# Kernel optimization log

Measured on AMD Instinct MI355X. Metric: run time of the kernel, lower is better.

The kernel has to match this reference:

```python
import jax, jax.numpy as jnp
import numpy as np

N, C, SI, VI, H, R = 10000, 2, 128, 16, 4, 32
SH, VH = SI // H, VI // H  # 32, 4
EPS = 1e-8

def _vnorm(x, axis):
    # clamped L2 norm, matches _norm_no_nan
    return jnp.sqrt(jnp.clip(jnp.sum(x * x, axis=axis), EPS, None))

def _gvp_full(s, v, wh, ws_w, ws_b, wv, wsv_w, wsv_b):
    # GVP with activations=(silu, sigmoid), vector_gate=True, vi=vo
    vh = jnp.swapaxes(v, -1, -2) @ wh            # [..., 3, h]
    vn = _vnorm(vh, -2)                          # [..., h]
    so = jnp.concatenate([s, vn], -1) @ ws_w + ws_b
    vo = jnp.swapaxes(vh @ wv, -1, -2)           # [..., vo, 3]
    gate = jax.nn.sigmoid(jax.nn.sigmoid(so) @ wsv_w + wsv_b)
    return jax.nn.silu(so), vo * gate[..., None]

def setup_inputs():
    key = jax.random.key(0)
    ks = iter(jax.random.split(key, 40))
    def lin(i, o):
        return jax.random.normal(next(ks), (i, o), jnp.float32) / np.sqrt(i)
    def bias(o):
        return 0.02 * jax.random.normal(next(ks), (o,), jnp.float32)
    inp = {}
    inp['s'] = jax.random.normal(next(ks), (N, C, SI), jnp.float32)
    inp['v'] = jax.random.normal(next(ks), (N, C, VI, 3), jnp.float32)
    # weight_proj: GVP((SI,VI)->(R,0)), no activations; h_dim = max(VI,0) = VI
    inp['wp_wh'] = lin(VI, VI); inp['wp_ws_w'] = lin(VI + SI, R); inp['wp_ws_b'] = bias(R)
    # to_q/k/v: GVP((SI,VI)->(SI,VI)), silu/sigmoid, vector_gate; h_dim = VI
    for p in ('q', 'k', 'vv'):
        inp[p + '_wh'] = lin(VI, VI)
        inp[p + '_ws_w'] = lin(VI + SI, SI); inp[p + '_ws_b'] = bias(SI)
        inp[p + '_wv'] = lin(VI, VI)
        inp[p + '_wsv_w'] = lin(SI, VI); inp[p + '_wsv_b'] = bias(VI)
    # attn_gvp_long: GVP((2*SH, 2*VH) -> (1,0)), no activations; h_dim = 2*VH
    inp['attn_wh'] = lin(2 * VH, 2 * VH)
    inp['attn_ws_w'] = lin(2 * VH + 2 * SH, 1); inp['attn_ws_b'] = bias(1)
    return inp

def reference(s, v, wp_wh, wp_ws_w, wp_ws_b,
              q_wh, q_ws_w, q_ws_b, q_wv, q_wsv_w, q_wsv_b,
              k_wh, k_ws_w, k_ws_b, k_wv, k_wsv_w, k_wsv_b,
              vv_wh, vv_ws_w, vv_ws_b, vv_wv, vv_wsv_w, vv_wsv_b,
              attn_wh, attn_ws_w, attn_ws_b):
    n, c = s.shape[:2]
    # ---- Compress: softmax-pool N -> R anchors ----
    vh = jnp.swapaxes(v, -1, -2) @ wp_wh          # [N,C,3,VI]
    vn = _vnorm(vh, -2)                            # [N,C,VI]
    pw = jnp.concatenate([s, vn], -1) @ wp_ws_w + wp_ws_b  # [N,C,R]
    pw = jax.nn.softmax(pw, axis=0)                # softmax over nodes
    s_g = jnp.einsum('nca,ncs->acs', pw, s)        # [R,C,SI] (includes transpose(0,1))
    v_g = jnp.einsum('nca,ncvd->acvd', pw, v)      # [R,C,VI,3]
    # ---- q from nodes, k/v from anchors ----
    qs, qv = _gvp_full(s, v, q_wh, q_ws_w, q_ws_b, q_wv, q_wsv_w, q_wsv_b)
    ks, kv = _gvp_full(s_g, v_g, k_wh, k_ws_w, k_ws_b, k_wv, k_wsv_w, k_wsv_b)
    vs, vv_ = _gvp_full(s_g, v_g, vv_wh, vv_ws_w, vv_ws_b, vv_wv, vv_wsv_w, vv_wsv_b)
    qs = qs.reshape(n, c, H, SH); qv = qv.reshape(n, c, H, VH, 3)
    ks = ks.reshape(R, c, H, SH); kv = kv.reshape(R, c, H, VH, 3)
    vs = vs.reshape(R, c, H, SH); vv_ = vv_.reshape(R, c, H, VH, 3)
    # ---- attention GVP on cat(q, k): split weights instead of materializing concat ----
    wh_q, wh_k = attn_wh[:VH], attn_wh[VH:]        # wh @ cat(qv,kv) = qv@wh_q + kv@wh_k
    qh = jnp.swapaxes(qv, -1, -2) @ wh_q           # [N,C,H,3,2VH]
    kh = jnp.swapaxes(kv, -1, -2) @ wh_k           # [R,C,H,3,2VH]
    vn2 = _vnorm(qh[:, None] + kh[None], -2)       # [N,R,C,H,2VH]
    ws_q = attn_ws_w[:SH]; ws_k = attn_ws_w[SH:2 * SH]; ws_n = attn_ws_w[2 * SH:]
    e = (qs @ ws_q)[:, None] + (ks @ ws_k)[None] + vn2 @ ws_n + attn_ws_b  # [N,R,C,H,1]
    e = e[..., 0] / np.sqrt(SH)
    alpha = jax.nn.softmax(e, axis=1)              # softmax over anchors (dim=1)
    # ---- Broadcast: weighted sum of anchor values ----
    out_s = jnp.einsum('nrch,rchd->nchd', alpha, vs).reshape(n, c, SI)
    out_v = jnp.einsum('nrch,rchde->nchde', alpha, vv_).reshape(n, c, VI, 3)
    return out_s, out_v
```

## Files before the change

### kernel.cpp

```cpp
#include <hip/hip_runtime.h>
#include <hip/hip_bf16.h>


#define N_  10000
#define C_  2
#define SI_ 128
#define VI_ 16
#define H_  4
#define R_  32
#define SH_ 32
#define VH_ 4
#define NC_ (N_*C_)

typedef const float* __restrict__ fptr;

__device__ __forceinline__ float sigm(float x){ return 1.f/(1.f+__expf(-x)); }

#define OFF_LG   0
#define OFF_EQH  640000
#define OFF_SG   2640000
#define OFF_TKH  2651520
#define OFF_TEK  2657664
#define OFF_TVS  2657920
#define OFF_TVV  2666112

#define SGSTRIDE_ 180

__global__ __launch_bounds__(256) void kA(
    fptr s, fptr v,
    fptr wp_wh, fptr wp_ws_w, fptr wp_ws_b,
    fptr q_wh, fptr q_ws_w, fptr q_ws_b, fptr q_wv, fptr q_wsv_w, fptr q_wsv_b,
    fptr attn_wh, fptr attn_ws_w,
    float* __restrict__ pexp, float* __restrict__ eqh)
{
  __shared__ __align__(16) float ARENA[160*20];
  __shared__ __align__(16) float VVs[16*48];
  __shared__ __align__(16) float VHQ[16*48];
  __shared__ __align__(16) float SO[16*128];
  __shared__ __align__(16) float GATE[16*16];
  __shared__ __align__(16) float QV[16*48];
  float* const XT  = ARENA;
  float* const SIG = ARENA;

  const int tid  = threadIdx.x;
  const int row0 = blockIdx.x * 16;

  for (int idx = tid; idx < 16*128; idx += 256){
    int r = idx >> 7, j = idx & 127;
    XT[j*20 + r] = s[(row0+r)*128 + j];
  }
  for (int idx = tid; idx < 16*48; idx += 256){
    int r = idx / 48, k = idx - r*48;
    VVs[r*48 + k] = v[(row0+r)*48 + k];
  }
  __syncthreads();

  for (int t = tid; t < 512; t += 256){
    int r = t >> 5, ii = t & 31, path = ii >> 4, i = ii & 15;
    fptr wh = path ? wp_wh : q_wh;
    float h0=0.f, h1=0.f, h2=0.f;
    #pragma unroll
    for (int j = 0; j < 16; j++){
      float w = wh[j*16 + i];
      h0 = fmaf(VVs[r*48 + j*3 + 0], w, h0);
      h1 = fmaf(VVs[r*48 + j*3 + 1], w, h1);
      h2 = fmaf(VVs[r*48 + j*3 + 2], w, h2);
    }
    float vn = sqrtf(fmaxf(h0*h0 + h1*h1 + h2*h2, 1e-8f));
    if (!path){
      VHQ[r*48 +  0 + i] = h0;
      VHQ[r*48 + 16 + i] = h1;
      VHQ[r*48 + 32 + i] = h2;
      XT[(128+i)*20 + r] = vn;
    } else {
      XT[(144+i)*20 + r] = vn;
    }
  }
  __syncthreads();

  const int colA = tid & 127, rgA = tid >> 7;
  float acc[8];
  {
    float bqs = q_ws_b[colA];
    #pragma unroll
    for (int k = 0; k < 8; k++) acc[k] = bqs;
    #pragma unroll 4
    for (int j = 0; j < 144; j++){
      float w = q_ws_w[j*128 + colA];
      const float* xp = &XT[j*20 + rgA*8];
      float4 x0 = *(const float4*)xp;
      float4 x1 = *(const float4*)(xp + 4);
      acc[0] = fmaf(x0.x, w, acc[0]); acc[1] = fmaf(x0.y, w, acc[1]);
      acc[2] = fmaf(x0.z, w, acc[2]); acc[3] = fmaf(x0.w, w, acc[3]);
      acc[4] = fmaf(x1.x, w, acc[4]); acc[5] = fmaf(x1.y, w, acc[5]);
      acc[6] = fmaf(x1.z, w, acc[6]); acc[7] = fmaf(x1.w, w, acc[7]);
    }
  }
  {
    const int col = tid & 31, rg = tid >> 5;
    float bp = wp_ws_b[col];
    float a0 = bp, a1 = bp;
    #pragma unroll 4
    for (int j = 0; j < 144; j++){
      int jj = (j < 128) ? j : (j + 16);
      float w = wp_ws_w[j*32 + col];
      const float* xp = &XT[jj*20 + rg*2];
      a0 = fmaf(xp[0], w, a0);
      a1 = fmaf(xp[1], w, a1);
    }
    const int n = (row0 >> 1) + rg;
    pexp[(     col)*N_ + n] = __expf(a0);
    pexp[(32 + col)*N_ + n] = __expf(a1);
  }
  __syncthreads();

  #pragma unroll
  for (int k = 0; k < 8; k++){
    float so = acc[k];
    float sg_ = sigm(so);
    SIG[(rgA*8 + k)*128 + colA] = sg_;
    SO [(rgA*8 + k)*128 + colA] = so * sg_;
  }
  __syncthreads();

  {
    const int r = tid >> 4, g = tid & 15;
    float ga = q_wsv_b[g];
    #pragma unroll 8
    for (int o = 0; o < 128; o += 4){
      float4 s4 = *(const float4*)&SIG[r*128 + o];
      ga = fmaf(s4.x, q_wsv_w[(o+0)*16 + g], ga);
      ga = fmaf(s4.y, q_wsv_w[(o+1)*16 + g], ga);
      ga = fmaf(s4.z, q_wsv_w[(o+2)*16 + g], ga);
      ga = fmaf(s4.w, q_wsv_w[(o+3)*16 + g], ga);
    }
    GATE[r*16 + g] = sigm(ga);
  }
  if (tid < 64){
    const int r = tid >> 2, h = tid & 3;
    float e = 0.f;
    #pragma unroll
    for (int t = 0; t < 32; t++)
      e = fmaf(SO[r*128 + h*32 + t], attn_ws_w[t], e);
    eqh[(row0 + r)*100 + h] = e;
  }
  __syncthreads();

  for (int t = tid; t < 16*48; t += 256){
    int r = t / 48, k = t - r*48, i = k / 3, d = k - i*3;
    float a = 0.f;
    #pragma unroll
    for (int j = 0; j < 16; j++)
      a = fmaf(VHQ[r*48 + d*16 + j], q_wv[j*16 + i], a);
    QV[r*48 + k] = a * GATE[r*16 + i];
  }
  __syncthreads();

  for (int t = tid; t < 16*96; t += 256){
    int r = t / 96, k = t - r*96;
    int h = k / 24, rem = k - h*24, d = rem >> 3, ee = rem & 7;
    float a = 0.f;
    #pragma unroll
    for (int i = 0; i < 4; i++)
      a = fmaf(QV[r*48 + (h*4 + i)*3 + d], attn_wh[i*8 + ee], a);
    eqh[(row0 + r)*100 + 8 + k] = a;
  }
}

__global__ __launch_bounds__(256) void kAccum(const float* __restrict__ pexp,
                                              fptr s, fptr v,
                                              float* __restrict__ sg)
{
  const int b = blockIdx.x;
  const int c = b & 1, ah = (b >> 1) & 1, chunk = b >> 2;
  const int n0 = chunk * 50;
  const int tid = threadIdx.x;
  const int ag = tid >> 6, dl = tid & 63;
  const int abase = ah*16 + ag*4;

  const float* pb = pexp + (c*32 + abase)*N_;
  float acc[4][3] = {};
  float dn[4] = {};

  #pragma unroll 2
  for (int n = n0; n < n0 + 50; n++){
    const int rc = n*2 + c;
    float pw[4];
    #pragma unroll
    for (int aa = 0; aa < 4; aa++){
      pw[aa] = pb[aa*N_ + n];
      dn[aa] += pw[aa];
    }
    #pragma unroll
    for (int dd = 0; dd < 3; dd++){
      int d = dl + 64*dd;
      if (d < 176){
        float xv = (d < 128) ? s[rc*128 + d] : v[rc*48 + d - 128];
        #pragma unroll
        for (int aa = 0; aa < 4; aa++)
          acc[aa][dd] = fmaf(pw[aa], xv, acc[aa][dd]);
      }
    }
  }
  #pragma unroll
  for (int aa = 0; aa < 4; aa++){
    const int base = (c*32 + abase + aa)*SGSTRIDE_;
    #pragma unroll
    for (int dd = 0; dd < 3; dd++){
      int d = dl + 64*dd;
      if (d < 176) atomicAdd(&sg[base + d], acc[aa][dd]);
    }
    if (dl == 0) atomicAdd(&sg[base + 176], dn[aa]);
  }
}

__global__ __launch_bounds__(256) void kSmall(
    const float* __restrict__ sg,
    fptr k_wh, fptr k_ws_w, fptr k_ws_b, fptr k_wv, fptr k_wsv_w, fptr k_wsv_b,
    fptr vv_wh, fptr vv_ws_w, fptr vv_ws_b, fptr vv_wv, fptr vv_wsv_w, fptr vv_wsv_b,
    fptr attn_wh, fptr attn_ws_w,
    float* __restrict__ tkh, float* __restrict__ tek,
    float* __restrict__ tvs, float* __restrict__ tvv)
{
  const int b = blockIdx.x, r = b >> 1, c = b & 1;
  const int tid = threadIdx.x;
  __shared__ float X[176];
  __shared__ float VN[2][16];
  __shared__ float VH[2][48];
  __shared__ float SOk[128], SOv[128];
  __shared__ float G[2][16];
  __shared__ float KV[48];

  if (tid < 176){
    const float* p = sg + (c*32 + r)*SGSTRIDE_;
    X[tid] = p[tid] / p[176];
  }
  __syncthreads();

  if (tid < 32){
    int path = tid >> 4, i = tid & 15;
    fptr wh = path ? vv_wh : k_wh;
    float h0=0.f, h1=0.f, h2=0.f;
    #pragma unroll
    for (int j = 0; j < 16; j++){
      float w = wh[j*16 + i];
      h0 = fmaf(X[128 + j*3 + 0], w, h0);
      h1 = fmaf(X[128 + j*3 + 1], w, h1);
      h2 = fmaf(X[128 + j*3 + 2], w, h2);
    }
    VH[path][ 0 + i] = h0; VH[path][16 + i] = h1; VH[path][32 + i] = h2;
    VN[path][i] = sqrtf(fmaxf(h0*h0 + h1*h1 + h2*h2, 1e-8f));
  }
  __syncthreads();

  {
    int path = tid >> 7, col = tid & 127;
    fptr W  = path ? vv_ws_w : k_ws_w;
    fptr Bb = path ? vv_ws_b : k_ws_b;
    float so = Bb[col];
    for (int j = 0; j < 128; j++) so = fmaf(X[j], W[j*128 + col], so);
    #pragma unroll
    for (int i = 0; i < 16; i++)  so = fmaf(VN[path][i], W[(128+i)*128 + col], so);
    (path ? SOv : SOk)[col] = so;
  }
  __syncthreads();

  if (tid < 32){
    int path = tid >> 4, g = tid & 15;
    fptr Wsv = path ? vv_wsv_w : k_wsv_w;
    fptr Bsv = path ? vv_wsv_b : k_wsv_b;
    const float* SOp = path ? SOv : SOk;
    float ga = Bsv[g];
    for (int o = 0; o < 128; o++)
      ga = fmaf(sigm(SOp[o]), Wsv[o*16 + g], ga);
    G[path][g] = sigm(ga);
  } else if (tid < 36){
    int h = tid - 32;
    float e = 0.f;
    #pragma unroll
    for (int t = 0; t < 32; t++){
      float so = SOk[h*32 + t];
      e = fmaf(so * sigm(so), attn_ws_w[32 + t], e);
    }
    tek[(r*2 + c)*4 + h] = e;
  } else if (tid >= 64 && tid < 192){
    int o = tid - 64;
    float so = SOv[o];
    tvs[(r*2 + c)*128 + o] = so * sigm(so);
  }
  __syncthreads();

  if (tid < 96){
    int path = tid / 48, k = tid % 48, i = k / 3, d = k - i*3;
    fptr Wv = path ? vv_wv : k_wv;
    float vo = 0.f;
    #pragma unroll
    for (int j = 0; j < 16; j++)
      vo = fmaf(VH[path][d*16 + j], Wv[j*16 + i], vo);
    float gv = vo * G[path][i];
    if (path == 0) KV[k] = gv;
    else {
      int h = i >> 2, ii = i & 3;
      tvv[(((r*2 + c)*4 + h)*4 + ii)*3 + d] = gv;
    }
  }
  __syncthreads();

  if (tid < 96){
    int h = tid / 24, rem = tid % 24, d = rem >> 3, ee = rem & 7;
    float a = 0.f;
    #pragma unroll
    for (int i = 0; i < 4; i++)
      a = fmaf(KV[(h*4 + i)*3 + d], attn_wh[(4 + i)*8 + ee], a);
    tkh[((r*2 + c)*4 + h)*24 + d*8 + ee] = a;
  }
}

__global__ __launch_bounds__(512, 1) void kAttn(
    const float* __restrict__ eqh,
    const float* __restrict__ tkh, const float* __restrict__ tek,
    const float* __restrict__ tvs, const float* __restrict__ tvv,
    fptr attn_ws_w, fptr attn_ws_b,
    float* __restrict__ out)
{
  __shared__ __align__(16) float KH[6144];
  __shared__ __align__(16) float EK[256];
  __shared__ __align__(16) float VS[256*36];
  __shared__ __align__(16) float VVt[3072];
  const int tid = threadIdx.x;

  for (int i = tid; i < 6144; i += 512) KH[i] = tkh[i];
  if (tid < 256) EK[tid] = tek[tid];
  for (int i = tid; i < 8192; i += 512){ int base = i >> 5, t = i & 31; VS[base*36 + t] = tvs[i]; }
  for (int i = tid; i < 3072; i += 512) VVt[i] = tvv[i];

  float wsn[8];
  #pragma unroll
  for (int ee = 0; ee < 8; ee++) wsn[ee] = attn_ws_w[64 + ee];
  const float wb = attn_ws_b[0];
  __syncthreads();

  const int row = blockIdx.x*128 + (tid >> 2);
  const int h = tid & 3;
  if (row < NC_){
    const int c = row & 1;
    const float eq = eqh[row*100 + h];
    float qh[24];
    {
      const float4* qp = (const float4*)&eqh[row*100 + 8 + h*24];
      #pragma unroll
      for (int k = 0; k < 6; k++){
        float4 t4 = qp[k];
        qh[k*4+0] = t4.x; qh[k*4+1] = t4.y; qh[k*4+2] = t4.z; qh[k*4+3] = t4.w;
      }
    }
    float4 accs4[8];
    float4 accv4[3];
    #pragma unroll
    for (int q = 0; q < 8; q++) accs4[q] = make_float4(0.f,0.f,0.f,0.f);
    #pragma unroll
    for (int q = 0; q < 3; q++) accv4[q] = make_float4(0.f,0.f,0.f,0.f);
    float den = 0.f;

    #pragma unroll
    for (int r = 0; r < 32; r++){
      const int base = (r*2 + c)*4 + h;
      const float* khp = &KH[base*24];
      float en = 0.f;
      #pragma unroll
      for (int ee = 0; ee < 8; ee++){
        float a0 = qh[ee]      + khp[ee];
        float a1 = qh[8 + ee]  + khp[8 + ee];
        float a2 = qh[16 + ee] + khp[16 + ee];
        en = fmaf(sqrtf(fmaxf(a0*a0 + a1*a1 + a2*a2, 1e-8f)), wsn[ee], en);
      }
      const float w = __expf((eq + EK[base] + en + wb) * 0.17677669529663687f);
      den += w;
      const float4* vp4 = (const float4*)&VS[base*36];
      #pragma unroll
      for (int q = 0; q < 8; q++){
        float4 t4 = vp4[q];
        accs4[q].x = fmaf(w, t4.x, accs4[q].x);
        accs4[q].y = fmaf(w, t4.y, accs4[q].y);
        accs4[q].z = fmaf(w, t4.z, accs4[q].z);
        accs4[q].w = fmaf(w, t4.w, accs4[q].w);
      }
      const float4* vv4 = (const float4*)&VVt[base*12];
      #pragma unroll
      for (int q = 0; q < 3; q++){
        float4 t4 = vv4[q];
        accv4[q].x = fmaf(w, t4.x, accv4[q].x);
        accv4[q].y = fmaf(w, t4.y, accv4[q].y);
        accv4[q].z = fmaf(w, t4.z, accv4[q].z);
        accv4[q].w = fmaf(w, t4.w, accv4[q].w);
      }
    }
    const float inv = 1.f / den;
    float4* po = (float4*)&out[row*128 + h*32];
    #pragma unroll
    for (int q = 0; q < 8; q++){
      float4 t4 = accs4[q];
      t4.x *= inv; t4.y *= inv; t4.z *= inv; t4.w *= inv;
      po[q] = t4;
    }
    float4* pv = (float4*)&out[NC_*128 + row*48 + h*12];
    #pragma unroll
    for (int q = 0; q < 3; q++){
      float4 t4 = accv4[q];
      t4.x *= inv; t4.y *= inv; t4.z *= inv; t4.w *= inv;
      pv[q] = t4;
    }
  }
}

extern "C" void kernel_launch(void* const* d_in, const int* in_sizes, int n_in,
                              void* d_out, int out_size, void* d_ws, size_t ws_size,
                              hipStream_t stream)
{
  fptr s        = (fptr)d_in[0];
  fptr v        = (fptr)d_in[1];
  fptr wp_wh    = (fptr)d_in[2];
  fptr wp_ws_w  = (fptr)d_in[3];
  fptr wp_ws_b  = (fptr)d_in[4];
  fptr q_wh     = (fptr)d_in[5];
  fptr q_ws_w   = (fptr)d_in[6];
  fptr q_ws_b   = (fptr)d_in[7];
  fptr q_wv     = (fptr)d_in[8];
  fptr q_wsv_w  = (fptr)d_in[9];
  fptr q_wsv_b  = (fptr)d_in[10];
  fptr k_wh     = (fptr)d_in[11];
  fptr k_ws_w   = (fptr)d_in[12];
  fptr k_ws_b   = (fptr)d_in[13];
  fptr k_wv     = (fptr)d_in[14];
  fptr k_wsv_w  = (fptr)d_in[15];
  fptr k_wsv_b  = (fptr)d_in[16];
  fptr vv_wh    = (fptr)d_in[17];
  fptr vv_ws_w  = (fptr)d_in[18];
  fptr vv_ws_b  = (fptr)d_in[19];
  fptr vv_wv    = (fptr)d_in[20];
  fptr vv_wsv_w = (fptr)d_in[21];
  fptr vv_wsv_b = (fptr)d_in[22];
  fptr attn_wh  = (fptr)d_in[23];
  fptr attn_ws_w= (fptr)d_in[24];
  fptr attn_ws_b= (fptr)d_in[25];

  float* ws   = (float*)d_ws;
  float* pexp = ws + OFF_LG;
  float* eqh  = ws + OFF_EQH;
  float* sg   = ws + OFF_SG;
  float* tkh  = ws + OFF_TKH;
  float* tek  = ws + OFF_TEK;
  float* tvs  = ws + OFF_TVS;
  float* tvv  = ws + OFF_TVV;

  hipMemsetAsync(sg, 0, 64*SGSTRIDE_*sizeof(float), stream);

  kA<<<NC_/16, 256, 0, stream>>>(s, v, wp_wh, wp_ws_w, wp_ws_b,
                                 q_wh, q_ws_w, q_ws_b, q_wv, q_wsv_w, q_wsv_b,
                                 attn_wh, attn_ws_w, pexp, eqh);
  kAccum<<<800, 256, 0, stream>>>(pexp, s, v, sg);
  kSmall<<<64, 256, 0, stream>>>(sg,
                                 k_wh, k_ws_w, k_ws_b, k_wv, k_wsv_w, k_wsv_b,
                                 vv_wh, vv_ws_w, vv_ws_b, vv_wv, vv_wsv_w, vv_wsv_b,
                                 attn_wh, attn_ws_w, tkh, tek, tvs, tvv);
  kAttn<<<(NC_ + 127)/128, 512, 0, stream>>>(eqh, tkh, tek, tvs, tvv,
                                             attn_ws_w, attn_ws_b, (float*)d_out);
}
```

Baseline: 244.8 us.

## Halve kA rows per block and fold sg zeroing into kA

The first kernel now processes 8 rows per block instead of 16, which doubles the grid to 2500 blocks and spreads the work across more CUs. Each thread keeps fewer accumulators, and the projection path is remapped so one thread handles one row. The separate hipMemsetAsync launch is removed and block 0 of kA zeroes the sg accumulator instead. In exchange, each q_ws_w and wp_ws_w weight load is amortised over fewer rows, so total weight traffic through the cache goes up.

```diff
diff --git a/kernel.cpp b/kernel.cpp
--- a/kernel.cpp
+++ b/kernel.cpp
@@ -31,32 +31,37 @@
     fptr wp_wh, fptr wp_ws_w, fptr wp_ws_b,
     fptr q_wh, fptr q_ws_w, fptr q_ws_b, fptr q_wv, fptr q_wsv_w, fptr q_wsv_b,
     fptr attn_wh, fptr attn_ws_w,
-    float* __restrict__ pexp, float* __restrict__ eqh)
+    float* __restrict__ pexp, float* __restrict__ eqh,
+    float* __restrict__ sgz)
 {
-  __shared__ __align__(16) float ARENA[160*20];
-  __shared__ __align__(16) float VVs[16*48];
-  __shared__ __align__(16) float VHQ[16*48];
-  __shared__ __align__(16) float SO[16*128];
-  __shared__ __align__(16) float GATE[16*16];
-  __shared__ __align__(16) float QV[16*48];
+  __shared__ __align__(16) float ARENA[160*12];
+  __shared__ __align__(16) float VVs[8*48];
+  __shared__ __align__(16) float VHQ[8*48];
+  __shared__ __align__(16) float SO[8*128];
+  __shared__ __align__(16) float GATE[8*16];
+  __shared__ __align__(16) float QV[8*48];
   float* const XT  = ARENA;
   float* const SIG = ARENA;
 
   const int tid  = threadIdx.x;
-  const int row0 = blockIdx.x * 16;
-
-  for (int idx = tid; idx < 16*128; idx += 256){
+  const int row0 = blockIdx.x * 8;
+
+  if (blockIdx.x == 0){
+    for (int i = tid; i < 64*SGSTRIDE_; i += 256) sgz[i] = 0.f;
+  }
+
+  for (int idx = tid; idx < 8*128; idx += 256){
     int r = idx >> 7, j = idx & 127;
-    XT[j*20 + r] = s[(row0+r)*128 + j];
-  }
-  for (int idx = tid; idx < 16*48; idx += 256){
+    XT[j*12 + r] = s[(row0+r)*128 + j];
+  }
+  for (int idx = tid; idx < 8*48; idx += 256){
     int r = idx / 48, k = idx - r*48;
     VVs[r*48 + k] = v[(row0+r)*48 + k];
   }
   __syncthreads();
 
-  for (int t = tid; t < 512; t += 256){
-    int r = t >> 5, ii = t & 31, path = ii >> 4, i = ii & 15;
+  {
+    int r = tid >> 5, ii = tid & 31, path = ii >> 4, i = ii & 15;
     fptr wh = path ? wp_wh : q_wh;
     float h0=0.f, h1=0.f, h2=0.f;
     #pragma unroll
@@ -71,59 +76,50 @@
       VHQ[r*48 +  0 + i] = h0;
       VHQ[r*48 + 16 + i] = h1;
       VHQ[r*48 + 32 + i] = h2;
-      XT[(128+i)*20 + r] = vn;
+      XT[(128+i)*12 + r] = vn;
     } else {
-      XT[(144+i)*20 + r] = vn;
+      XT[(144+i)*12 + r] = vn;
     }
   }
   __syncthreads();
 
   const int colA = tid & 127, rgA = tid >> 7;
-  float acc[8];
+  float acc[4];
   {
     float bqs = q_ws_b[colA];
     #pragma unroll
-    for (int k = 0; k < 8; k++) acc[k] = bqs;
-    #pragma unroll 4
+    for (int k = 0; k < 4; k++) acc[k] = bqs;
+    #pragma unroll 8
     for (int j = 0; j < 144; j++){
       float w = q_ws_w[j*128 + colA];
-      const float* xp = &XT[j*20 + rgA*8];
-      float4 x0 = *(const float4*)xp;
-      float4 x1 = *(const float4*)(xp + 4);
+      float4 x0 = *(const float4*)&XT[j*12 + rgA*4];
       acc[0] = fmaf(x0.x, w, acc[0]); acc[1] = fmaf(x0.y, w, acc[1]);
       acc[2] = fmaf(x0.z, w, acc[2]); acc[3] = fmaf(x0.w, w, acc[3]);
-      acc[4] = fmaf(x1.x, w, acc[4]); acc[5] = fmaf(x1.y, w, acc[5]);
-      acc[6] = fmaf(x1.z, w, acc[6]); acc[7] = fmaf(x1.w, w, acc[7]);
     }
   }
   {
     const int col = tid & 31, rg = tid >> 5;
-    float bp = wp_ws_b[col];
-    float a0 = bp, a1 = bp;
-    #pragma unroll 4
+    float a0 = wp_ws_b[col];
+    #pragma unroll 8
     for (int j = 0; j < 144; j++){
       int jj = (j < 128) ? j : (j + 16);
-      float w = wp_ws_w[j*32 + col];
-      const float* xp = &XT[jj*20 + rg*2];
-      a0 = fmaf(xp[0], w, a0);
-      a1 = fmaf(xp[1], w, a1);
-    }
-    const int n = (row0 >> 1) + rg;
-    pexp[(     col)*N_ + n] = __expf(a0);
-    pexp[(32 + col)*N_ + n] = __expf(a1);
+      a0 = fmaf(XT[jj*12 + rg], wp_ws_w[j*32 + col], a0);
+    }
+    const int c = rg & 1, n = (row0 + rg) >> 1;
+    pexp[(c*32 + col)*N_ + n] = __expf(a0);
   }
   __syncthreads();
 
   #pragma unroll
-  for (int k = 0; k < 8; k++){
+  for (int k = 0; k < 4; k++){
     float so = acc[k];
     float sg_ = sigm(so);
-    SIG[(rgA*8 + k)*128 + colA] = sg_;
-    SO [(rgA*8 + k)*128 + colA] = so * sg_;
-  }
-  __syncthreads();
-
-  {
+    SIG[(rgA*4 + k)*128 + colA] = sg_;
+    SO [(rgA*4 + k)*128 + colA] = so * sg_;
+  }
+  __syncthreads();
+
+  if (tid < 128){
     const int r = tid >> 4, g = tid & 15;
     float ga = q_wsv_b[g];
     #pragma unroll 8
@@ -135,9 +131,8 @@
       ga = fmaf(s4.w, q_wsv_w[(o+3)*16 + g], ga);
     }
     GATE[r*16 + g] = sigm(ga);
-  }
-  if (tid < 64){
-    const int r = tid >> 2, h = tid & 3;
+  } else if (tid < 160){
+    const int t2 = tid - 128, r = t2 >> 2, h = t2 & 3;
     float e = 0.f;
     #pragma unroll
     for (int t = 0; t < 32; t++)
@@ -146,7 +141,7 @@
   }
   __syncthreads();
 
-  for (int t = tid; t < 16*48; t += 256){
+  for (int t = tid; t < 8*48; t += 256){
     int r = t / 48, k = t - r*48, i = k / 3, d = k - i*3;
     float a = 0.f;
     #pragma unroll
@@ -156,7 +151,7 @@
   }
   __syncthreads();
 
-  for (int t = tid; t < 16*96; t += 256){
+  for (int t = tid; t < 8*96; t += 256){
     int r = t / 96, k = t - r*96;
     int h = k / 24, rem = k - h*24, d = rem >> 3, ee = rem & 7;
     float a = 0.f;
@@ -453,11 +448,9 @@
   float* tvs  = ws + OFF_TVS;
   float* tvv  = ws + OFF_TVV;
 
-  hipMemsetAsync(sg, 0, 64*SGSTRIDE_*sizeof(float), stream);
-
-  kA<<<NC_/16, 256, 0, stream>>>(s, v, wp_wh, wp_ws_w, wp_ws_b,
-                                 q_wh, q_ws_w, q_ws_b, q_wv, q_wsv_w, q_wsv_b,
-                                 attn_wh, attn_ws_w, pexp, eqh);
+  kA<<<NC_/8, 256, 0, stream>>>(s, v, wp_wh, wp_ws_w, wp_ws_b,
+                                q_wh, q_ws_w, q_ws_b, q_wv, q_wsv_w, q_wsv_b,
+                                attn_wh, attn_ws_w, pexp, eqh, sg);
   kAccum<<<800, 256, 0, stream>>>(pexp, s, v, sg);
   kSmall<<<64, 256, 0, stream>>>(sg,
                                  k_wh, k_ws_w, k_ws_b, k_wv, k_wsv_w, k_wsv_b,
```

Measured after the change: 240.8 us. No clear change (-1.6%).
